# Performance work log

Measured on AMD Instinct MI355X. Metric: run time of the kernel, lower is better.

The kernel has to match this reference:

```python
import jax, jax.numpy as jnp
import numpy as np

TEMP = 0.5
ALPHA, BETA, GAMMA, LAMBDA = 1e-3, 5e-4, 1e-3, 5e-6
LN_EPS = 1e-5


def _attention(x, temp):
    # x: [N,C,H,W]
    N, C, H, W = x.shape
    v = jnp.abs(x)
    fea = v.mean(axis=1)                                   # [N,H,W] mean over channels
    S = (H * W) * jax.nn.softmax((fea / temp).reshape(N, -1), axis=1)
    S = S.reshape(N, H, W)
    ch = v.mean(axis=(2, 3))                               # [N,C]
    Catt = C * jax.nn.softmax(ch / temp, axis=1)
    return S, Catt


def _masks(gt, img_h, img_w, H, W):
    # gt: [N,nt,4] (x1,y1,x2,y2) in input-image pixels; rescale to feature grid
    sw = W / img_w
    sh = H / img_h
    wmin = jnp.floor(gt[..., 0] * sw)                      # [N,nt]
    wmax = jnp.ceil(gt[..., 2] * sw)
    hmin = jnp.floor(gt[..., 1] * sh)
    hmax = jnp.ceil(gt[..., 3] * sh)
    area = 1.0 / ((hmax + 1.0 - hmin) * (wmax + 1.0 - wmin))  # [N,nt]
    hs = jnp.arange(H, dtype=gt.dtype)
    ws = jnp.arange(W, dtype=gt.dtype)
    in_h = (hs[None, None, :] >= hmin[..., None]) & (hs[None, None, :] <= hmax[..., None])  # [N,nt,H]
    in_w = (ws[None, None, :] >= wmin[..., None]) & (ws[None, None, :] <= wmax[..., None])  # [N,nt,W]
    inside = in_h[:, :, :, None] & in_w[:, :, None, :]     # [N,nt,H,W]
    # scatter-max over boxes, starting from zeros (matches in-place torch.maximum loop)
    Mask_fg = jnp.max(jnp.where(inside, area[:, :, None, None], 0.0), axis=1)  # [N,H,W]
    Mask_bg = jnp.where(Mask_fg > 0, 0.0, 1.0)
    s = Mask_bg.sum(axis=(1, 2), keepdims=True)
    Mask_bg = jnp.where(s > 0, Mask_bg / s, Mask_bg)
    return Mask_fg, Mask_bg


def _spatial_pool(x, w, b):
    # GC-block context: w [1,C], b [1]
    N, C, H, W = x.shape
    cm = jnp.einsum('oc,nchw->nhw', w, x).reshape(N, H * W) + b[0]
    cm = jax.nn.softmax(cm, axis=1)                        # [N,HW]
    ctx = jnp.einsum('nck,nk->nc', x.reshape(N, C, H * W), cm)
    return ctx                                             # [N,C]


def _channel_add(ctx, w1, b1, lnw, lnb, w2, b2):
    y = ctx @ w1.T + b1                                    # [N,C/2]
    mu = y.mean(axis=-1, keepdims=True)
    var = y.var(axis=-1, keepdims=True)                    # biased var, like nn.LayerNorm
    y = (y - mu) / jnp.sqrt(var + LN_EPS) * lnw + lnb
    y = jax.nn.relu(y)
    return y @ w2.T + b2                                   # [N,C]


def _fgd_loss(preds_S, preds_T, gt_bboxes, cms_w, cms_b, cmt_w, cmt_b,
              cas_w1, cas_b1, cas_lnw, cas_lnb, cas_w2, cas_b2,
              cat_w1, cat_b1, cat_lnw, cat_lnb, cat_w2, cat_b2, img_h, img_w):
    N, C, H, W = preds_S.shape
    S_t, C_t = _attention(preds_T, TEMP)
    S_s, C_s = _attention(preds_S, TEMP)
    Mask_fg, Mask_bg = _masks(gt_bboxes, img_h, img_w, H, W)
    mfg = Mask_fg[:, None]                                 # [N,1,H,W]
    mbg = Mask_bg[:, None]
    fg_loss = jnp.sum((preds_S * mfg - preds_T * mfg) ** 2) / N
    bg_loss = jnp.sum((preds_S * mbg - preds_T * mbg) ** 2) / N
    mask_loss = jnp.sum(jnp.abs(C_s - C_t)) / N + jnp.sum(jnp.abs(S_s - S_t)) / N
    ctx_s = _spatial_pool(preds_S, cms_w, cms_b)
    ctx_t = _spatial_pool(preds_T, cmt_w, cmt_b)
    out_s = preds_S + _channel_add(ctx_s, cas_w1, cas_b1, cas_lnw, cas_lnb, cas_w2, cas_b2)[:, :, None, None]
    out_t = preds_T + _channel_add(ctx_t, cat_w1, cat_b1, cat_lnw, cat_lnb, cat_w2, cat_b2)[:, :, None, None]
    rela_loss = jnp.sum((out_s - out_t) ** 2) / N
    return ALPHA * fg_loss + BETA * bg_loss + GAMMA * mask_loss + LAMBDA * rela_loss


def setup_inputs() -> dict:
    key = jax.random.key(0)
    ks = jax.random.split(key, 16)
    N, C, H, W, NT = 8, 256, 100, 152, 20
    IMG_H, IMG_W = 800, 1216
    preds_S = jax.random.normal(ks[0], (N, C, H, W), dtype=jnp.float32)
    preds_T = jax.random.normal(ks[1], (N, C, H, W), dtype=jnp.float32)
    # boxes: two random corners per box, sorted -> valid (x1,y1,x2,y2) in image pixels
    p1 = jax.random.uniform(ks[2], (N, NT, 2))
    p2 = jax.random.uniform(ks[3], (N, NT, 2))
    lo = jnp.minimum(p1, p2)
    hi = jnp.maximum(p1, p2)
    scale = jnp.array([IMG_W, IMG_H], dtype=jnp.float32)
    gt_bboxes = jnp.concatenate([lo * scale, hi * scale], axis=-1)  # [N,NT,4]
    C2 = C // 2
    s = 0.02
    return {
        'preds_S': preds_S, 'preds_T': preds_T, 'gt_bboxes': gt_bboxes,
        'cms_w': jax.random.normal(ks[4], (1, C)) * s, 'cms_b': jnp.zeros((1,), jnp.float32),
        'cmt_w': jax.random.normal(ks[5], (1, C)) * s, 'cmt_b': jnp.zeros((1,), jnp.float32),
        'cas_w1': jax.random.normal(ks[6], (C2, C)) * s, 'cas_b1': jnp.zeros((C2,), jnp.float32),
        'cas_lnw': jnp.ones((C2,), jnp.float32), 'cas_lnb': jnp.zeros((C2,), jnp.float32),
        'cas_w2': jax.random.normal(ks[7], (C, C2)) * s, 'cas_b2': jnp.zeros((C,), jnp.float32),
        'cat_w1': jax.random.normal(ks[8], (C2, C)) * s, 'cat_b1': jnp.zeros((C2,), jnp.float32),
        'cat_lnw': jnp.ones((C2,), jnp.float32), 'cat_lnb': jnp.zeros((C2,), jnp.float32),
        'cat_w2': jax.random.normal(ks[9], (C, C2)) * s, 'cat_b2': jnp.zeros((C,), jnp.float32),
        'img_h': 800, 'img_w': 1216,
    }


def reference(preds_S, preds_T, gt_bboxes, cms_w, cms_b, cmt_w, cmt_b,
              cas_w1, cas_b1, cas_lnw, cas_lnb, cas_w2, cas_b2,
              cat_w1, cat_b1, cat_lnw, cat_lnb, cat_w2, cat_b2, img_h, img_w):
    return _fgd_loss(preds_S, preds_T, gt_bboxes, cms_w, cms_b, cmt_w, cmt_b,
                     cas_w1, cas_b1, cas_lnw, cas_lnb, cas_w2, cas_b2,
                     cat_w1, cat_b1, cat_lnw, cat_lnb, cat_w2, cat_b2, img_h, img_w)
```

## Files before the change

kernel.cpp:

```cpp
#include <hip/hip_runtime.h>

#define N_    8
#define C_    256
#define H_    100
#define W_    152
#define HW_   (H_*W_)
#define NHW_  (N_*HW_)
#define NT_   20
#define TEMP_ 0.5f
#define LN_EPS_ 1e-5f
#define PB_   ((HW_+255)/256)

#define PXB1_ 256
#define NSEG1_ 60
#define NCHK_ 4
#define CHK_  64
#define NB1_  (N_*NSEG1_*NCHK_)

#define PXS_  950
#define NSEGS_ 16

__device__ __forceinline__ float wred_sum(float v){
#pragma unroll
  for(int o=32;o;o>>=1) v += __shfl_xor(v,o,64);
  return v;
}
__device__ __forceinline__ float wred_max(float v){
#pragma unroll
  for(int o=32;o;o>>=1) v = fmaxf(v,__shfl_xor(v,o,64));
  return v;
}
__device__ float block_sum(float v, float* sm){
  v = wred_sum(v);
  int nw = (int)(blockDim.x>>6);
  __syncthreads();
  if((threadIdx.x&63)==0) sm[threadIdx.x>>6]=v;
  __syncthreads();
  float r=0.f;
  for(int i=0;i<nw;i++) r+=sm[i];
  return r;
}
__device__ float block_max(float v, float* sm){
  v = wred_max(v);
  int nw = (int)(blockDim.x>>6);
  __syncthreads();
  if((threadIdx.x&63)==0) sm[threadIdx.x>>6]=v;
  __syncthreads();
  float r=-3.4e38f;
  for(int i=0;i<nw;i++) r=fmaxf(r,sm[i]);
  return r;
}

__global__ void k_masks(const float* __restrict__ gt, const int* __restrict__ imh,
                        const int* __restrict__ imw,
                        float* __restrict__ mask_fg, float* __restrict__ acc){
  __shared__ float sm[16];
  int b = blockIdx.x;
  int n = b / PB_;
  int pp = (b % PB_)*256 + threadIdx.x;
  float sw = (float)W_ / (float)imw[0];
  float sh = (float)H_ / (float)imh[0];
  float fg = 0.f;
  bool valid = pp < HW_;
  if (valid){
    float hh = (float)(pp / W_);
    float ww = (float)(pp % W_);
#pragma unroll
    for(int t=0;t<NT_;t++){
      const float* bx = gt + ((size_t)(n*NT_)+t)*4;
      float wmin = floorf(bx[0]*sw);
      float hmin = floorf(bx[1]*sh);
      float wmax = ceilf (bx[2]*sw);
      float hmax = ceilf (bx[3]*sh);
      float area = 1.f/((hmax+1.f-hmin)*(wmax+1.f-wmin));
      bool in = (hh>=hmin)&&(hh<=hmax)&&(ww>=wmin)&&(ww<=wmax);
      fg = fmaxf(fg, in?area:0.f);
    }
    mask_fg[n*HW_+pp] = fg;
  }
  float bgf = (valid && fg<=0.f) ? 1.f : 0.f;
  float s = block_sum(bgf, sm);
  if(threadIdx.x==0) atomicAdd(&acc[6+n], s);
}

__global__ void __launch_bounds__(256, 8) k_pass1(
    const float* __restrict__ S, const float* __restrict__ T,
    const float* __restrict__ ws_w, const float* __restrict__ wt_w,
    const float* __restrict__ mask_fg,
    float* __restrict__ part, float* __restrict__ pblk,
    const float* __restrict__ acc){
  __shared__ float accw[4][4][PXB1_];
  __shared__ float m2fg[PXB1_], m2bg[PXB1_];
  __shared__ float lw_s[CHK_], lw_t[CHK_];
  __shared__ float sm[8];
  int b = blockIdx.x;
  int cc = b & (NCHK_-1);
  int sg = (b>>2) % NSEG1_;
  int n  = b/(NCHK_*NSEG1_);
  int tid = threadIdx.x, wv = tid>>6, ln = tid&63;
  int c0 = cc*CHK_;
  int px0 = sg*PXB1_;
  size_t base = (size_t)n*HW_ + px0;
  if(tid<CHK_){ lw_s[tid]=ws_w[c0+tid]; lw_t[tid]=wt_w[c0+tid]; }
  {
    float bgc = acc[6+n];
    float ibg = (bgc>0.f)?(1.f/bgc):1.f;
    float ibg2 = ibg*ibg;
    if(tid < PXB1_){
      if(px0 + tid < HW_){
        float m = mask_fg[base+tid];
        m2fg[tid] = m*m;
        m2bg[tid] = (m<=0.f)? ibg2 : 0.f;
      } else { m2fg[tid]=0.f; m2bg[tid]=0.f; }
    }
  }
#pragma unroll
  for(int q=0;q<4;q++){
    for(int idx=ln; idx<PXB1_; idx+=64) accw[wv][q][idx]=0.f;
  }
  __syncthreads();
  float wfg=0.f, wbg=0.f, wd2=0.f;
  for(int ci=0;ci<16;ci++){
    int c = c0 + wv*16 + ci;
    const float2* Sp = (const float2*)(S + (size_t)(n*C_+c)*HW_ + px0);
    const float2* Tp = (const float2*)(T + (size_t)(n*C_+c)*HW_ + px0);
    float wsv = lw_s[wv*16+ci], wtv = lw_t[wv*16+ci];
#pragma unroll
    for(int i=0;i<2;i++){
      int slot = i*64 + ln;
      int px = slot*2;
      if(px0 + px < HW_){
        float2 s2 = Sp[slot];
        float2 t2 = Tp[slot];
        float2* a0 = (float2*)&accw[wv][0][px];
        float2* a1 = (float2*)&accw[wv][1][px];
        float2* a2 = (float2*)&accw[wv][2][px];
        float2* a3 = (float2*)&accw[wv][3][px];
        float2 v0=*a0, v1=*a1, v2=*a2, v3=*a3;
        v0.x += fabsf(s2.x); v0.y += fabsf(s2.y);
        v1.x += fabsf(t2.x); v1.y += fabsf(t2.y);
        v2.x += wsv*s2.x;    v2.y += wsv*s2.y;
        v3.x += wtv*t2.x;    v3.y += wtv*t2.y;
        *a0=v0; *a1=v1; *a2=v2; *a3=v3;
        float d0 = s2.x-t2.x, d1 = s2.y-t2.y;
        float d0s = d0*d0, d1s = d1*d1;
        wfg += m2fg[px]*d0s + m2fg[px+1]*d1s;
        wbg += m2bg[px]*d0s + m2bg[px+1]*d1s;
        wd2 += d0s + d1s;
      }
    }
  }
  __syncthreads();
  if(px0 + tid < HW_){
#pragma unroll
    for(int q=0;q<4;q++){
      float r = accw[0][q][tid]+accw[1][q][tid]+accw[2][q][tid]+accw[3][q][tid];
      part[(size_t)(q*NCHK_+cc)*NHW_ + base + tid] = r;
    }
  }
  float s1 = block_sum(wfg, sm);
  float s2 = block_sum(wbg, sm);
  float s3 = block_sum(wd2, sm);
  if(tid==0){
    pblk[0*NB1_+b]=s1; pblk[1*NB1_+b]=s2; pblk[2*NB1_+b]=s3;
  }
}

__global__ void k_scal(const float* __restrict__ pblk, float* __restrict__ acc){
  __shared__ float sm[4];
  int q = blockIdx.x, tid = threadIdx.x;
  float v=0.f;
  for(int i=tid;i<NB1_;i+=256) v += pblk[q*NB1_+i];
  float s = block_sum(v, sm);
  if(tid==0) acc[q]=s;
}

__global__ void __launch_bounds__(256) k_combA(float* __restrict__ part,
                                               float* __restrict__ mpart){
  __shared__ float sm[8];
  int b = blockIdx.x;
  int q = b>>7, n = (b>>4)&7, seg = b&15;
  int tid = threadIdx.x;
  size_t off = (size_t)n*HW_ + seg*PXS_;
  float*       p0 = part + (size_t)(q*NCHK_+0)*NHW_ + off;
  const float* p1 = part + (size_t)(q*NCHK_+1)*NHW_ + off;
  const float* p2 = part + (size_t)(q*NCHK_+2)*NHW_ + off;
  const float* p3 = part + (size_t)(q*NCHK_+3)*NHW_ + off;
  float mloc = -3.4e38f;
  for(int i=tid;i<PXS_;i+=256){
    float w = p0[i]+p1[i]+p2[i]+p3[i];
    p0[i]=w;
    mloc = fmaxf(mloc,w);
  }
  float m = block_max(mloc,sm);
  if(tid==0) mpart[(q*8+n)*NSEGS_+seg]=m;
}

__global__ void k_sp2(const float* __restrict__ mpart, float* __restrict__ macc){
  int t=threadIdx.x;
  if(t<32){
    float m=-3.4e38f;
    for(int s=0;s<NSEGS_;s++) m=fmaxf(m,mpart[t*NSEGS_+s]);
    macc[t]=m;
  }
}

__global__ void __launch_bounds__(256) k_sp3(const float* __restrict__ part,
                                             const float* __restrict__ macc,
                                             float* __restrict__ zpart){
  __shared__ float sm[8];
  int b = blockIdx.x;
  int q = b>>7, n = (b>>4)&7, seg = b&15;
  int tid = threadIdx.x;
  const float* p0 = part + (size_t)(q*NCHK_)*NHW_ + (size_t)n*HW_ + seg*PXS_;
  float m = macc[q*8+n];
  const float invf = 1.f/((float)C_*TEMP_);
  float z=0.f;
  for(int i=tid;i<PXS_;i+=256){
    float v = p0[i];
    z += (q<2)? expf((v-m)*invf) : expf(v-m);
  }
  z = block_sum(z,sm);
  if(tid==0) zpart[(q*8+n)*NSEGS_+seg]=z;
}

__global__ void __launch_bounds__(256) k_sp4(float* __restrict__ part,
                                             const float* __restrict__ macc,
                                             const float* __restrict__ zpart,
                                             float* __restrict__ acc){
  __shared__ float zz[4];
  __shared__ float sm[8];
  int b = blockIdx.x;
  int n = b>>4, seg = b&15;
  int tid = threadIdx.x;
  if(tid<4){
    float z=0.f;
    for(int s=0;s<NSEGS_;s++) z += zpart[(tid*8+n)*NSEGS_+s];
    zz[tid]=z;
  }
  __syncthreads();
  float m1=macc[0*8+n], m2=macc[1*8+n], m3=macc[2*8+n], m4=macc[3*8+n];
  float i1=(float)HW_/zz[0], i2=(float)HW_/zz[1], i3=1.f/zz[2], i4=1.f/zz[3];
  size_t off = (size_t)n*HW_ + seg*PXS_;
  const float* fs = part + (size_t)(0*NCHK_)*NHW_ + off;
  const float* ft = part + (size_t)(1*NCHK_)*NHW_ + off;
  float* cs = part + (size_t)(2*NCHK_)*NHW_ + off;
  float* ct = part + (size_t)(3*NCHK_)*NHW_ + off;
  const float invf = 1.f/((float)C_*TEMP_);
  float d=0.f;
  for(int i=tid;i<PXS_;i+=256){
    float Ss = expf((fs[i]-m1)*invf)*i1;
    float St = expf((ft[i]-m2)*invf)*i2;
    d += fabsf(Ss-St);
    cs[i] = expf(cs[i]-m3)*i3;
    ct[i] = expf(ct[i]-m4)*i4;
  }
  d = block_sum(d,sm);
  if(tid==0) atomicAdd(&acc[3], d);
}

__global__ void __launch_bounds__(256) k_pass2(
    const float* __restrict__ S, const float* __restrict__ T,
    const float* __restrict__ cmp_s, const float* __restrict__ cmp_t,
    float* __restrict__ ctx_s, float* __restrict__ ctx_t,
    float* __restrict__ ch_s, float* __restrict__ ch_t,
    float* __restrict__ sum_d){
  __shared__ float sm[16];
  int b=blockIdx.x;
  int n=b>>8, c=b&255;
  const float4* Sp = (const float4*)(S + (size_t)(n*C_+c)*HW_);
  const float4* Tp = (const float4*)(T + (size_t)(n*C_+c)*HW_);
  const float4* Pp = (const float4*)(cmp_s + (size_t)n*HW_);
  const float4* Qp = (const float4*)(cmp_t + (size_t)n*HW_);
  float as=0.f, at=0.f, dd=0.f, xs=0.f, xt=0.f;
  const int HWE = HW_/8;
  for(int p=threadIdx.x;p<HWE;p+=256){
    float4 s0=Sp[p], s1=Sp[p+HWE];
    float4 t0=Tp[p], t1=Tp[p+HWE];
    float4 u0=Pp[p], u1=Pp[p+HWE];
    float4 v0=Qp[p], v1=Qp[p+HWE];
    as += fabsf(s0.x)+fabsf(s0.y)+fabsf(s0.z)+fabsf(s0.w)
        + fabsf(s1.x)+fabsf(s1.y)+fabsf(s1.z)+fabsf(s1.w);
    at += fabsf(t0.x)+fabsf(t0.y)+fabsf(t0.z)+fabsf(t0.w)
        + fabsf(t1.x)+fabsf(t1.y)+fabsf(t1.z)+fabsf(t1.w);
    dd += (s0.x-t0.x)+(s0.y-t0.y)+(s0.z-t0.z)+(s0.w-t0.w)
        + (s1.x-t1.x)+(s1.y-t1.y)+(s1.z-t1.z)+(s1.w-t1.w);
    xs += s0.x*u0.x+s0.y*u0.y+s0.z*u0.z+s0.w*u0.w
        + s1.x*u1.x+s1.y*u1.y+s1.z*u1.z+s1.w*u1.w;
    xt += t0.x*v0.x+t0.y*v0.y+t0.z*v0.z+t0.w*v0.w
        + t1.x*v1.x+t1.y*v1.y+t1.z*v1.z+t1.w*v1.w;
  }
  as = block_sum(as,sm);
  at = block_sum(at,sm);
  dd = block_sum(dd,sm);
  xs = block_sum(xs,sm);
  xt = block_sum(xt,sm);
  if(threadIdx.x==0){
    ch_s[n*C_+c]=as; ch_t[n*C_+c]=at; sum_d[n*C_+c]=dd;
    ctx_s[n*C_+c]=xs; ctx_t[n*C_+c]=xt;
  }
}

__global__ void k_tw(const float* __restrict__ sw1, const float* __restrict__ tw1,
                     const float* __restrict__ sw2, const float* __restrict__ tw2,
                     float* __restrict__ o){
  int g = blockIdx.x;
  int which = g>>7;
  int i = (g&127)*256 + threadIdx.x;
  const float* src = (which==0)?sw1 : (which==1)?tw1 : (which==2)?sw2 : tw2;
  int Ccols = (which<2)?256:128;
  int Rrows = (which<2)?128:256;
  int r = i/Ccols, c = i%Ccols;
  o[which*32768 + c*Rrows + r] = src[i];
}

__global__ void k_chcadd(const float* __restrict__ ch_s, const float* __restrict__ ch_t,
    const float* __restrict__ ctx_s, const float* __restrict__ ctx_t,
    const float* __restrict__ wT,
    const float* __restrict__ sb1, const float* __restrict__ slnw, const float* __restrict__ slnb,
    const float* __restrict__ sb2,
    const float* __restrict__ tb1, const float* __restrict__ tlnw, const float* __restrict__ tlnb,
    const float* __restrict__ tb2,
    const float* __restrict__ sum_d, float* __restrict__ acc){
  __shared__ float sm[16];
  __shared__ float sred[8];
  __shared__ float lcs[C_], lct[C_], lh[C_];
  int n=blockIdx.x, tid=threadIdx.x;
  {
    const float invc = 1.f/((float)HW_*TEMP_);
    float vs = ch_s[n*C_+tid]*invc;
    float vt = ch_t[n*C_+tid]*invc;
    float ms = block_max(vs,sm);
    float mt = block_max(vt,sm);
    float es = expf(vs-ms), et = expf(vt-mt);
    float zs = block_sum(es,sm), zt = block_sum(et,sm);
    float Cs = (float)C_*es/zs, Ct = (float)C_*et/zt;
    float d = block_sum(fabsf(Cs-Ct), sm);
    if(tid==0) atomicAdd(&acc[4], d);
  }
  const float* w1T_s = wT;
  const float* w1T_t = wT + 32768;
  const float* w2T_s = wT + 65536;
  const float* w2T_t = wT + 98304;
  lcs[tid]=ctx_s[n*C_+tid]; lct[tid]=ctx_t[n*C_+tid];
  __syncthreads();
  int half = tid>>7, k = tid&127;
  float y;
  {
    const float* w1T = half? w1T_t : w1T_s;
    const float* b1  = half? tb1 : sb1;
    const float* src = half? lct : lcs;
    float a = b1[k];
    for(int c=0;c<C_;c++) a += src[c]*w1T[c*128+k];
    y = a;
  }
  {
    int wv = tid>>6;
    float s1 = wred_sum(y);
    float s2 = wred_sum(y*y);
    __syncthreads();
    if((tid&63)==0){ sred[wv]=s1; sred[4+wv]=s2; }
    __syncthreads();
    int h2 = half<<1;
    float mu = (sred[h2]+sred[h2+1])*(1.f/128.f);
    float msq = (sred[4+h2]+sred[4+h2+1])*(1.f/128.f);
    float var = msq - mu*mu;
    const float* lnw = half? tlnw : slnw;
    const float* lnb = half? tlnb : slnb;
    float yv = (y-mu)/sqrtf(var+LN_EPS_)*lnw[k]+lnb[k];
    lh[tid] = fmaxf(yv, 0.f);
  }
  __syncthreads();
  {
    int c = tid;
    float os = sb2[c], ot = tb2[c];
    for(int kk=0;kk<128;kk++){
      os += lh[kk]*w2T_s[kk*256+c];
      ot += lh[128+kk]*w2T_t[kk*256+c];
    }
    float e = os - ot;
    float p = 2.f*e*sum_d[n*C_+c] + (float)HW_*e*e;
    float s = block_sum(p, sm);
    if(tid==0) atomicAdd(&acc[5], s);
  }
}

__global__ void k_final(const float* __restrict__ acc, float* __restrict__ out){
  if(threadIdx.x==0 && blockIdx.x==0){
    float fg=acc[0], bg=acc[1], d2=acc[2], mS=acc[3], mC=acc[4], rl=acc[5];
    const float invN = 1.f/(float)N_;
    out[0] = 0.001f*fg*invN + 0.0005f*bg*invN
           + 0.001f*(mC+mS)*invN + 5e-6f*(d2+rl)*invN;
  }
}

extern "C" void kernel_launch(void* const* d_in, const int* in_sizes, int n_in,
                              void* d_out, int out_size, void* d_ws, size_t ws_size,
                              hipStream_t stream){
  (void)in_sizes; (void)n_in; (void)out_size; (void)ws_size;
  const float* S     = (const float*)d_in[0];
  const float* T     = (const float*)d_in[1];
  const float* gt    = (const float*)d_in[2];
  const float* cms_w = (const float*)d_in[3];
  const float* cmt_w = (const float*)d_in[5];
  const float* cas_w1=(const float*)d_in[7],  *cas_b1=(const float*)d_in[8];
  const float* cas_lnw=(const float*)d_in[9], *cas_lnb=(const float*)d_in[10];
  const float* cas_w2=(const float*)d_in[11], *cas_b2=(const float*)d_in[12];
  const float* cat_w1=(const float*)d_in[13], *cat_b1=(const float*)d_in[14];
  const float* cat_lnw=(const float*)d_in[15],*cat_lnb=(const float*)d_in[16];
  const float* cat_w2=(const float*)d_in[17], *cat_b2=(const float*)d_in[18];
  const int* imh=(const int*)d_in[19];
  const int* imw=(const int*)d_in[20];

  float* ws = (float*)d_ws;
  const int NC = N_*C_;
  float* mask_fg = ws;
  float* part    = mask_fg + NHW_;
  float* pblk    = part + (size_t)4*NCHK_*NHW_;
  float* ctx_s   = pblk + 3*NB1_;
  float* ctx_t   = ctx_s + NC;
  float* ch_s    = ctx_t + NC;
  float* ch_t    = ch_s + NC;
  float* sum_d   = ch_t + NC;
  float* wT      = sum_d + NC;
  float* acc     = wT + 4*32768;
  float* mpart   = acc + 16;
  float* zpart   = mpart + 512;
  float* macc    = zpart + 512;
  hipMemsetAsync(acc, 0, 16*sizeof(float), stream);

  float* cmp_s = part + (size_t)2*NCHK_*NHW_;
  float* cmp_t = part + (size_t)3*NCHK_*NHW_;

  k_tw    <<<512,        256, 0, stream>>>(cas_w1,cat_w1,cas_w2,cat_w2, wT);
  k_masks <<<N_*PB_,     256, 0, stream>>>(gt, imh, imw, mask_fg, acc);
  k_pass1 <<<NB1_,       256, 0, stream>>>(S,T,cms_w,cmt_w,mask_fg, part, pblk, acc);
  k_scal  <<<3,          256, 0, stream>>>(pblk, acc);
  k_combA <<<512,        256, 0, stream>>>(part, mpart);
  k_sp2   <<<1,           64, 0, stream>>>(mpart, macc);
  k_sp3   <<<512,        256, 0, stream>>>(part, macc, zpart);
  k_sp4   <<<128,        256, 0, stream>>>(part, macc, zpart, acc);
  k_pass2 <<<N_*C_,      256, 0, stream>>>(S,T,cmp_s,cmp_t,
                                           ctx_s,ctx_t,ch_s,ch_t,sum_d);
  k_chcadd<<<N_,         256, 0, stream>>>(ch_s,ch_t, ctx_s,ctx_t, wT,
                                           cas_b1,cas_lnw,cas_lnb,cas_b2,
                                           cat_b1,cat_lnw,cat_lnb,cat_b2,
                                           sum_d,acc);
  k_final <<<1,           64, 0, stream>>>(acc,(float*)d_out);
}
```

Measured before the change: 141.2 us.

## Move masked squared-diff sums into pass2 and split pass1 per tensor

The foreground, background and total squared-difference reductions move out of pass1 and into pass2, which already reads S and T in full. pass2 also reads the foreground mask, and a new scal2 kernel sums the per-block partials after pass2. pass1 now reads only one of S or T per block, with 1024 threads, each wave covering 4 channels, and accumulates channel-abs and context-weighted sums into shared memory with atomic adds. This removes the mask handling and the joint S/T read from pass1, making it lighter, but shared-memory atomics may contend, and launch order has to ensure acc[6+n] is final before pass2 runs.

```diff
diff --git a/kernel.cpp b/kernel.cpp
--- a/kernel.cpp
+++ b/kernel.cpp
@@ -10,12 +10,10 @@
 #define TEMP_ 0.5f
 #define LN_EPS_ 1e-5f
 #define PB_   ((HW_+255)/256)
-
-#define PXB1_ 256
-#define NSEG1_ 60
 #define NCHK_ 4
-#define CHK_  64
-#define NB1_  (N_*NSEG1_*NCHK_)
+
+#define EI_   1900
+#define NP2_  (N_*C_)
 
 #define PXS_  950
 #define NSEGS_ 16
@@ -83,96 +81,52 @@
   if(threadIdx.x==0) atomicAdd(&acc[6+n], s);
 }
 
-__global__ void __launch_bounds__(256, 8) k_pass1(
+__global__ void __launch_bounds__(1024) k_pass1(
     const float* __restrict__ S, const float* __restrict__ T,
     const float* __restrict__ ws_w, const float* __restrict__ wt_w,
-    const float* __restrict__ mask_fg,
-    float* __restrict__ part, float* __restrict__ pblk,
-    const float* __restrict__ acc){
-  __shared__ float accw[4][4][PXB1_];
-  __shared__ float m2fg[PXB1_], m2bg[PXB1_];
-  __shared__ float lw_s[CHK_], lw_t[CHK_];
-  __shared__ float sm[8];
+    float* __restrict__ part){
+  __shared__ float ac[2][EI_];
   int b = blockIdx.x;
-  int cc = b & (NCHK_-1);
-  int sg = (b>>2) % NSEG1_;
-  int n  = b/(NCHK_*NSEG1_);
+  int e  = b & 7;
+  int cc = (b>>3) & 3;
+  int n  = (b>>5) & 7;
+  int which = b>>8;
   int tid = threadIdx.x, wv = tid>>6, ln = tid&63;
-  int c0 = cc*CHK_;
-  int px0 = sg*PXB1_;
-  size_t base = (size_t)n*HW_ + px0;
-  if(tid<CHK_){ lw_s[tid]=ws_w[c0+tid]; lw_t[tid]=wt_w[c0+tid]; }
-  {
-    float bgc = acc[6+n];
-    float ibg = (bgc>0.f)?(1.f/bgc):1.f;
-    float ibg2 = ibg*ibg;
-    if(tid < PXB1_){
-      if(px0 + tid < HW_){
-        float m = mask_fg[base+tid];
-        m2fg[tid] = m*m;
-        m2bg[tid] = (m<=0.f)? ibg2 : 0.f;
-      } else { m2fg[tid]=0.f; m2bg[tid]=0.f; }
-    }
-  }
-#pragma unroll
-  for(int q=0;q<4;q++){
-    for(int idx=ln; idx<PXB1_; idx+=64) accw[wv][q][idx]=0.f;
-  }
-  __syncthreads();
-  float wfg=0.f, wbg=0.f, wd2=0.f;
-  for(int ci=0;ci<16;ci++){
-    int c = c0 + wv*16 + ci;
-    const float2* Sp = (const float2*)(S + (size_t)(n*C_+c)*HW_ + px0);
-    const float2* Tp = (const float2*)(T + (size_t)(n*C_+c)*HW_ + px0);
-    float wsv = lw_s[wv*16+ci], wtv = lw_t[wv*16+ci];
-#pragma unroll
-    for(int i=0;i<2;i++){
-      int slot = i*64 + ln;
-      int px = slot*2;
-      if(px0 + px < HW_){
-        float2 s2 = Sp[slot];
-        float2 t2 = Tp[slot];
-        float2* a0 = (float2*)&accw[wv][0][px];
-        float2* a1 = (float2*)&accw[wv][1][px];
-        float2* a2 = (float2*)&accw[wv][2][px];
-        float2* a3 = (float2*)&accw[wv][3][px];
-        float2 v0=*a0, v1=*a1, v2=*a2, v3=*a3;
-        v0.x += fabsf(s2.x); v0.y += fabsf(s2.y);
-        v1.x += fabsf(t2.x); v1.y += fabsf(t2.y);
-        v2.x += wsv*s2.x;    v2.y += wsv*s2.y;
-        v3.x += wtv*t2.x;    v3.y += wtv*t2.y;
-        *a0=v0; *a1=v1; *a2=v2; *a3=v3;
-        float d0 = s2.x-t2.x, d1 = s2.y-t2.y;
-        float d0s = d0*d0, d1s = d1*d1;
-        wfg += m2fg[px]*d0s + m2fg[px+1]*d1s;
-        wbg += m2bg[px]*d0s + m2bg[px+1]*d1s;
-        wd2 += d0s + d1s;
-      }
-    }
-  }
-  __syncthreads();
-  if(px0 + tid < HW_){
-#pragma unroll
-    for(int q=0;q<4;q++){
-      float r = accw[0][q][tid]+accw[1][q][tid]+accw[2][q][tid]+accw[3][q][tid];
-      part[(size_t)(q*NCHK_+cc)*NHW_ + base + tid] = r;
-    }
-  }
-  float s1 = block_sum(wfg, sm);
-  float s2 = block_sum(wbg, sm);
-  float s3 = block_sum(wd2, sm);
-  if(tid==0){
-    pblk[0*NB1_+b]=s1; pblk[1*NB1_+b]=s2; pblk[2*NB1_+b]=s3;
-  }
-}
-
-__global__ void k_scal(const float* __restrict__ pblk, float* __restrict__ acc){
-  __shared__ float sm[4];
-  int q = blockIdx.x, tid = threadIdx.x;
-  float v=0.f;
-  for(int i=tid;i<NB1_;i+=256) v += pblk[q*NB1_+i];
-  float s = block_sum(v, sm);
-  if(tid==0) acc[q]=s;
+  const float* X = which ? T : S;
+  const float* W = which ? wt_w : ws_w;
+  for(int i=tid;i<EI_;i+=1024){ ac[0][i]=0.f; ac[1][i]=0.f; }
+  __syncthreads();
+  int c = cc*64 + wv*4;
+  int px0 = e*EI_;
+  const float4* X0 = (const float4*)(X + (size_t)(n*C_+c+0)*HW_ + px0);
+  const float4* X1 = (const float4*)(X + (size_t)(n*C_+c+1)*HW_ + px0);
+  const float4* X2 = (const float4*)(X + (size_t)(n*C_+c+2)*HW_ + px0);
+  const float4* X3 = (const float4*)(X + (size_t)(n*C_+c+3)*HW_ + px0);
+  float w0=W[c], w1=W[c+1], w2=W[c+2], w3=W[c+3];
+  for(int i=ln; i<EI_/4; i+=64){
+    float4 a=X0[i], bb=X1[i], cq=X2[i], d=X3[i];
+    int px = i*4;
+    float f0 = fabsf(a.x)+fabsf(bb.x)+fabsf(cq.x)+fabsf(d.x);
+    float f1 = fabsf(a.y)+fabsf(bb.y)+fabsf(cq.y)+fabsf(d.y);
+    float f2 = fabsf(a.z)+fabsf(bb.z)+fabsf(cq.z)+fabsf(d.z);
+    float f3 = fabsf(a.w)+fabsf(bb.w)+fabsf(cq.w)+fabsf(d.w);
+    float g0 = w0*a.x+w1*bb.x+w2*cq.x+w3*d.x;
+    float g1 = w0*a.y+w1*bb.y+w2*cq.y+w3*d.y;
+    float g2 = w0*a.z+w1*bb.z+w2*cq.z+w3*d.z;
+    float g3 = w0*a.w+w1*bb.w+w2*cq.w+w3*d.w;
+    atomicAdd(&ac[0][px+0], f0); atomicAdd(&ac[0][px+1], f1);
+    atomicAdd(&ac[0][px+2], f2); atomicAdd(&ac[0][px+3], f3);
+    atomicAdd(&ac[1][px+0], g0); atomicAdd(&ac[1][px+1], g1);
+    atomicAdd(&ac[1][px+2], g2); atomicAdd(&ac[1][px+3], g3);
+  }
+  __syncthreads();
+  size_t off = (size_t)n*HW_ + px0;
+  int q_fea = which;
+  int q_cmp = 2+which;
+  for(int i=tid;i<EI_/4;i+=1024){
+    ((float4*)(part + (size_t)(q_fea*NCHK_+cc)*NHW_ + off))[i] = ((float4*)ac[0])[i];
+    ((float4*)(part + (size_t)(q_cmp*NCHK_+cc)*NHW_ + off))[i] = ((float4*)ac[1])[i];
+  }
 }
 
 __global__ void __launch_bounds__(256) k_combA(float* __restrict__ part,
@@ -262,9 +216,10 @@
 __global__ void __launch_bounds__(256) k_pass2(
     const float* __restrict__ S, const float* __restrict__ T,
     const float* __restrict__ cmp_s, const float* __restrict__ cmp_t,
+    const float* __restrict__ mask_fg, const float* __restrict__ acc,
     float* __restrict__ ctx_s, float* __restrict__ ctx_t,
     float* __restrict__ ch_s, float* __restrict__ ch_t,
-    float* __restrict__ sum_d){
+    float* __restrict__ sum_d, float* __restrict__ pblk2){
   __shared__ float sm[16];
   int b=blockIdx.x;
   int n=b>>8, c=b&255;
@@ -272,19 +227,35 @@
   const float4* Tp = (const float4*)(T + (size_t)(n*C_+c)*HW_);
   const float4* Pp = (const float4*)(cmp_s + (size_t)n*HW_);
   const float4* Qp = (const float4*)(cmp_t + (size_t)n*HW_);
+  const float4* Mp = (const float4*)(mask_fg + (size_t)n*HW_);
+  float bgc = acc[6+n];
+  float ibg = (bgc>0.f)?(1.f/bgc):1.f;
+  float ibg2 = ibg*ibg;
   float as=0.f, at=0.f, dd=0.f, xs=0.f, xt=0.f;
+  float wfg=0.f, wbg=0.f, wd2=0.f;
   const int HWE = HW_/8;
   for(int p=threadIdx.x;p<HWE;p+=256){
     float4 s0=Sp[p], s1=Sp[p+HWE];
     float4 t0=Tp[p], t1=Tp[p+HWE];
     float4 u0=Pp[p], u1=Pp[p+HWE];
     float4 v0=Qp[p], v1=Qp[p+HWE];
+    float4 m0=Mp[p], m1=Mp[p+HWE];
     as += fabsf(s0.x)+fabsf(s0.y)+fabsf(s0.z)+fabsf(s0.w)
         + fabsf(s1.x)+fabsf(s1.y)+fabsf(s1.z)+fabsf(s1.w);
     at += fabsf(t0.x)+fabsf(t0.y)+fabsf(t0.z)+fabsf(t0.w)
         + fabsf(t1.x)+fabsf(t1.y)+fabsf(t1.z)+fabsf(t1.w);
-    dd += (s0.x-t0.x)+(s0.y-t0.y)+(s0.z-t0.z)+(s0.w-t0.w)
-        + (s1.x-t1.x)+(s1.y-t1.y)+(s1.z-t1.z)+(s1.w-t1.w);
+    float d0x=s0.x-t0.x, d0y=s0.y-t0.y, d0z=s0.z-t0.z, d0w=s0.w-t0.w;
+    float d1x=s1.x-t1.x, d1y=s1.y-t1.y, d1z=s1.z-t1.z, d1w=s1.w-t1.w;
+    dd += d0x+d0y+d0z+d0w + d1x+d1y+d1z+d1w;
+    float q0x=d0x*d0x, q0y=d0y*d0y, q0z=d0z*d0z, q0w=d0w*d0w;
+    float q1x=d1x*d1x, q1y=d1y*d1y, q1z=d1z*d1z, q1w=d1w*d1w;
+    wd2 += q0x+q0y+q0z+q0w + q1x+q1y+q1z+q1w;
+    wfg += m0.x*m0.x*q0x + m0.y*m0.y*q0y + m0.z*m0.z*q0z + m0.w*m0.w*q0w
+         + m1.x*m1.x*q1x + m1.y*m1.y*q1y + m1.z*m1.z*q1z + m1.w*m1.w*q1w;
+    wbg += ((m0.x<=0.f)?ibg2:0.f)*q0x + ((m0.y<=0.f)?ibg2:0.f)*q0y
+         + ((m0.z<=0.f)?ibg2:0.f)*q0z + ((m0.w<=0.f)?ibg2:0.f)*q0w
+         + ((m1.x<=0.f)?ibg2:0.f)*q1x + ((m1.y<=0.f)?ibg2:0.f)*q1y
+         + ((m1.z<=0.f)?ibg2:0.f)*q1z + ((m1.w<=0.f)?ibg2:0.f)*q1w;
     xs += s0.x*u0.x+s0.y*u0.y+s0.z*u0.z+s0.w*u0.w
         + s1.x*u1.x+s1.y*u1.y+s1.z*u1.z+s1.w*u1.w;
     xt += t0.x*v0.x+t0.y*v0.y+t0.z*v0.z+t0.w*v0.w
@@ -295,10 +266,23 @@
   dd = block_sum(dd,sm);
   xs = block_sum(xs,sm);
   xt = block_sum(xt,sm);
+  wfg = block_sum(wfg,sm);
+  wbg = block_sum(wbg,sm);
+  wd2 = block_sum(wd2,sm);
   if(threadIdx.x==0){
     ch_s[n*C_+c]=as; ch_t[n*C_+c]=at; sum_d[n*C_+c]=dd;
     ctx_s[n*C_+c]=xs; ctx_t[n*C_+c]=xt;
-  }
+    pblk2[0*NP2_+b]=wfg; pblk2[1*NP2_+b]=wbg; pblk2[2*NP2_+b]=wd2;
+  }
+}
+
+__global__ void k_scal2(const float* __restrict__ pblk2, float* __restrict__ acc){
+  __shared__ float sm[4];
+  int q = blockIdx.x, tid = threadIdx.x;
+  float v=0.f;
+  for(int i=tid;i<NP2_;i+=256) v += pblk2[q*NP2_+i];
+  float s = block_sum(v, sm);
+  if(tid==0) acc[q]=s;
 }
 
 __global__ void k_tw(const float* __restrict__ sw1, const float* __restrict__ tw1,
@@ -416,8 +400,8 @@
   const int NC = N_*C_;
   float* mask_fg = ws;
   float* part    = mask_fg + NHW_;
-  float* pblk    = part + (size_t)4*NCHK_*NHW_;
-  float* ctx_s   = pblk + 3*NB1_;
+  float* pblk2   = part + (size_t)4*NCHK_*NHW_;
+  float* ctx_s   = pblk2 + 3*NP2_;
   float* ctx_t   = ctx_s + NC;
   float* ch_s    = ctx_t + NC;
   float* ch_t    = ch_s + NC;
@@ -434,14 +418,14 @@
 
   k_tw    <<<512,        256, 0, stream>>>(cas_w1,cat_w1,cas_w2,cat_w2, wT);
   k_masks <<<N_*PB_,     256, 0, stream>>>(gt, imh, imw, mask_fg, acc);
-  k_pass1 <<<NB1_,       256, 0, stream>>>(S,T,cms_w,cmt_w,mask_fg, part, pblk, acc);
-  k_scal  <<<3,          256, 0, stream>>>(pblk, acc);
+  k_pass1 <<<512,       1024, 0, stream>>>(S,T,cms_w,cmt_w, part);
   k_combA <<<512,        256, 0, stream>>>(part, mpart);
   k_sp2   <<<1,           64, 0, stream>>>(mpart, macc);
   k_sp3   <<<512,        256, 0, stream>>>(part, macc, zpart);
   k_sp4   <<<128,        256, 0, stream>>>(part, macc, zpart, acc);
-  k_pass2 <<<N_*C_,      256, 0, stream>>>(S,T,cmp_s,cmp_t,
-                                           ctx_s,ctx_t,ch_s,ch_t,sum_d);
+  k_pass2 <<<NP2_,       256, 0, stream>>>(S,T,cmp_s,cmp_t, mask_fg, acc,
+                                           ctx_s,ctx_t,ch_s,ch_t,sum_d, pblk2);
+  k_scal2 <<<3,          256, 0, stream>>>(pblk2, acc);
   k_chcadd<<<N_,         256, 0, stream>>>(ch_s,ch_t, ctx_s,ctx_t, wT,
                                            cas_b1,cas_lnw,cas_lnb,cas_b2,
                                            cat_b1,cat_lnw,cat_lnb,cat_b2,
```

Result: slower. 259.0 us (+83.5%).

## Restructure pass1 to per-pixel register accumulation with direct global-to-LDS staging

Applied to the files above, without the earlier changes.

The first pass now splits channels into two halves instead of four chunks and has each thread own one pixel, accumulating abs sums, context logits and squared differences in registers. Channel rows are staged into shared memory with direct global-to-LDS loads, 16 channels per stage. This removes the per-wave shared-memory read-modify-write accumulators and halves the partial buffers the combine kernel must sum. The last strip is shifted back to stay in bounds and its overlap is masked out of the scalar sums. Fewer blocks and two barriers per stage may reduce latency hiding.

```diff
diff --git a/kernel.cpp b/kernel.cpp
--- a/kernel.cpp
+++ b/kernel.cpp
@@ -11,14 +11,23 @@
 #define LN_EPS_ 1e-5f
 #define PB_   ((HW_+255)/256)
 
+#define NCHK_ 2
+#define HALFC_ 128
+#define STGC_ 16
+#define NSTG_ 8
 #define PXB1_ 256
-#define NSEG1_ 60
-#define NCHK_ 4
-#define CHK_  64
-#define NB1_  (N_*NSEG1_*NCHK_)
+#define NSTRP_ 60
+#define NB1_  (N_*NSTRP_*NCHK_)
+#define NP2_  (N_*C_)
 
 #define PXS_  950
 #define NSEGS_ 16
+
+__device__ __forceinline__ void gload_lds16(const float* g, float* l){
+  __builtin_amdgcn_global_load_lds(
+      (const __attribute__((address_space(1))) void*)(g),
+      (__attribute__((address_space(3))) void*)(l), 16, 0, 0);
+}
 
 __device__ __forceinline__ float wred_sum(float v){
 #pragma unroll
@@ -83,81 +92,69 @@
   if(threadIdx.x==0) atomicAdd(&acc[6+n], s);
 }
 
-__global__ void __launch_bounds__(256, 8) k_pass1(
+__global__ void __launch_bounds__(256) k_pass1(
     const float* __restrict__ S, const float* __restrict__ T,
     const float* __restrict__ ws_w, const float* __restrict__ wt_w,
     const float* __restrict__ mask_fg,
     float* __restrict__ part, float* __restrict__ pblk,
     const float* __restrict__ acc){
-  __shared__ float accw[4][4][PXB1_];
+  __shared__ float s16[STGC_][PXB1_];
+  __shared__ float t16[STGC_][PXB1_];
   __shared__ float m2fg[PXB1_], m2bg[PXB1_];
-  __shared__ float lw_s[CHK_], lw_t[CHK_];
+  __shared__ float lw_s[HALFC_], lw_t[HALFC_];
   __shared__ float sm[8];
   int b = blockIdx.x;
-  int cc = b & (NCHK_-1);
-  int sg = (b>>2) % NSEG1_;
-  int n  = b/(NCHK_*NSEG1_);
+  int half = b & 1;
+  int sg = (b>>1) % NSTRP_;
+  int n  = b/(NCHK_*NSTRP_);
   int tid = threadIdx.x, wv = tid>>6, ln = tid&63;
-  int c0 = cc*CHK_;
-  int px0 = sg*PXB1_;
+  int c0h = half*HALFC_;
+  int pv0 = sg*PXB1_;
+  int px0 = pv0;
+  if(px0 + PXB1_ > HW_) px0 = HW_ - PXB1_;
   size_t base = (size_t)n*HW_ + px0;
-  if(tid<CHK_){ lw_s[tid]=ws_w[c0+tid]; lw_t[tid]=wt_w[c0+tid]; }
+  if(tid < HALFC_){ lw_s[tid]=ws_w[c0h+tid]; lw_t[tid]=wt_w[c0h+tid]; }
   {
     float bgc = acc[6+n];
     float ibg = (bgc>0.f)?(1.f/bgc):1.f;
-    float ibg2 = ibg*ibg;
     if(tid < PXB1_){
-      if(px0 + tid < HW_){
-        float m = mask_fg[base+tid];
-        m2fg[tid] = m*m;
-        m2bg[tid] = (m<=0.f)? ibg2 : 0.f;
-      } else { m2fg[tid]=0.f; m2bg[tid]=0.f; }
+      float m = mask_fg[base+tid];
+      m2fg[tid] = m*m;
+      m2bg[tid] = (m<=0.f)? ibg*ibg : 0.f;
     }
   }
-#pragma unroll
-  for(int q=0;q<4;q++){
-    for(int idx=ln; idx<PXB1_; idx+=64) accw[wv][q][idx]=0.f;
-  }
-  __syncthreads();
-  float wfg=0.f, wbg=0.f, wd2=0.f;
-  for(int ci=0;ci<16;ci++){
-    int c = c0 + wv*16 + ci;
-    const float2* Sp = (const float2*)(S + (size_t)(n*C_+c)*HW_ + px0);
-    const float2* Tp = (const float2*)(T + (size_t)(n*C_+c)*HW_ + px0);
-    float wsv = lw_s[wv*16+ci], wtv = lw_t[wv*16+ci];
-#pragma unroll
-    for(int i=0;i<2;i++){
-      int slot = i*64 + ln;
-      int px = slot*2;
-      if(px0 + px < HW_){
-        float2 s2 = Sp[slot];
-        float2 t2 = Tp[slot];
-        float2* a0 = (float2*)&accw[wv][0][px];
-        float2* a1 = (float2*)&accw[wv][1][px];
-        float2* a2 = (float2*)&accw[wv][2][px];
-        float2* a3 = (float2*)&accw[wv][3][px];
-        float2 v0=*a0, v1=*a1, v2=*a2, v3=*a3;
-        v0.x += fabsf(s2.x); v0.y += fabsf(s2.y);
-        v1.x += fabsf(t2.x); v1.y += fabsf(t2.y);
-        v2.x += wsv*s2.x;    v2.y += wsv*s2.y;
-        v3.x += wtv*t2.x;    v3.y += wtv*t2.y;
-        *a0=v0; *a1=v1; *a2=v2; *a3=v3;
-        float d0 = s2.x-t2.x, d1 = s2.y-t2.y;
-        float d0s = d0*d0, d1s = d1*d1;
-        wfg += m2fg[px]*d0s + m2fg[px+1]*d1s;
-        wbg += m2bg[px]*d0s + m2bg[px+1]*d1s;
-        wd2 += d0s + d1s;
-      }
+  __syncthreads();
+  float fs=0.f, ft=0.f, cs=0.f, ct=0.f, d2=0.f;
+  for(int st=0; st<NSTG_; ++st){
+#pragma unroll
+    for(int r=0;r<4;++r){
+      int row = wv*4+r;
+      int c = c0h + st*STGC_ + row;
+      const float* gS = S + (size_t)(n*C_+c)*HW_ + px0 + ln*4;
+      const float* gT = T + (size_t)(n*C_+c)*HW_ + px0 + ln*4;
+      gload_lds16(gS, &s16[row][0]);
+      gload_lds16(gT, &t16[row][0]);
     }
-  }
-  __syncthreads();
-  if(px0 + tid < HW_){
-#pragma unroll
-    for(int q=0;q<4;q++){
-      float r = accw[0][q][tid]+accw[1][q][tid]+accw[2][q][tid]+accw[3][q][tid];
-      part[(size_t)(q*NCHK_+cc)*NHW_ + base + tid] = r;
+    __syncthreads();
+#pragma unroll
+    for(int c=0;c<STGC_;++c){
+      float sv = s16[c][tid];
+      float tv = t16[c][tid];
+      int ci = st*STGC_+c;
+      fs += fabsf(sv); ft += fabsf(tv);
+      cs += lw_s[ci]*sv; ct += lw_t[ci]*tv;
+      float d = sv-tv;  d2 += d*d;
     }
-  }
+    __syncthreads();
+  }
+  part[(size_t)(0*NCHK_+half)*NHW_ + base + tid] = fs;
+  part[(size_t)(1*NCHK_+half)*NHW_ + base + tid] = ft;
+  part[(size_t)(2*NCHK_+half)*NHW_ + base + tid] = cs;
+  part[(size_t)(3*NCHK_+half)*NHW_ + base + tid] = ct;
+  bool sval = (px0 + tid) >= pv0;
+  float wd2 = sval? d2 : 0.f;
+  float wfg = sval? m2fg[tid]*d2 : 0.f;
+  float wbg = sval? m2bg[tid]*d2 : 0.f;
   float s1 = block_sum(wfg, sm);
   float s2 = block_sum(wbg, sm);
   float s3 = block_sum(wd2, sm);
@@ -182,13 +179,12 @@
   int q = b>>7, n = (b>>4)&7, seg = b&15;
   int tid = threadIdx.x;
   size_t off = (size_t)n*HW_ + seg*PXS_;
-  float*       p0 = part + (size_t)(q*NCHK_+0)*NHW_ + off;
-  const float* p1 = part + (size_t)(q*NCHK_+1)*NHW_ + off;
-  const float* p2 = part + (size_t)(q*NCHK_+2)*NHW_ + off;
-  const float* p3 = part + (size_t)(q*NCHK_+3)*NHW_ + off;
+  float* p0 = part + (size_t)(q*NCHK_+0)*NHW_ + off;
   float mloc = -3.4e38f;
   for(int i=tid;i<PXS_;i+=256){
-    float w = p0[i]+p1[i]+p2[i]+p3[i];
+    float w = p0[i];
+#pragma unroll
+    for(int c=1;c<NCHK_;c++) w += (part + (size_t)(q*NCHK_+c)*NHW_ + off)[i];
     p0[i]=w;
     mloc = fmaxf(mloc,w);
   }
@@ -440,7 +436,7 @@
   k_sp2   <<<1,           64, 0, stream>>>(mpart, macc);
   k_sp3   <<<512,        256, 0, stream>>>(part, macc, zpart);
   k_sp4   <<<128,        256, 0, stream>>>(part, macc, zpart, acc);
-  k_pass2 <<<N_*C_,      256, 0, stream>>>(S,T,cmp_s,cmp_t,
+  k_pass2 <<<NP2_,       256, 0, stream>>>(S,T,cmp_s,cmp_t,
                                            ctx_s,ctx_t,ch_s,ch_t,sum_d);
   k_chcadd<<<N_,         256, 0, stream>>>(ch_s,ch_t, ctx_s,ctx_t, wT,
                                            cas_b1,cas_lnw,cas_lnb,cas_b2,
```

Result: no change. 138.8 us (-1.7%).
